# Kernel optimization log

Measured on AMD Instinct MI355X. Metric: run time of the kernel, lower is better.

## Reference

```python
import jax, jax.numpy as jnp
import numpy as np

N_ATOM, N_FRAG, N_EDGE, N_FEDGE, N_MEM = 131072, 32768, 262144, 65536, 196608
B, H, IN_A, IN_F, IN_E, L, OUT = 4096, 256, 64, 32, 16, 4, 1


def setup_inputs():
    ks = iter(jax.random.split(jax.random.key(0), 96))

    def nrm(shape, s=0.05):
        return jax.random.normal(next(ks), shape, jnp.float32) * s

    def ri(shape, hi):
        return jax.random.randint(next(ks), shape, 0, hi)

    z = lambda *s: jnp.zeros(s, jnp.float32)
    o = lambda *s: jnp.ones(s, jnp.float32)
    return {
        'x': nrm((N_ATOM, IN_A), 1.0),
        'fragments': nrm((N_FRAG, IN_F), 1.0),
        'edge_attr': nrm((N_EDGE, IN_E), 1.0),
        'atom_enc_W': nrm((IN_A, H)), 'atom_enc_b': z(H),
        'frag_enc_W': nrm((IN_F, H)), 'frag_enc_b': z(H),
        'bond_W': nrm((L, IN_E, H)), 'bond_b': z(L, H),
        'gine_eps': z(L),
        'gine_W1': nrm((L, H, 2 * H)), 'gine_b1': z(L, 2 * H),
        'gine_bn_g': o(L, 2 * H), 'gine_bn_b': z(L, 2 * H),
        'gine_W2': nrm((L, 2 * H, H)), 'gine_b2': z(L, H),
        'atom_bn_g': o(L, H), 'atom_bn_b': z(L, H),
        'gin_eps': z(L),
        'gin_W1': nrm((L, H, 2 * H)), 'gin_b1': z(L, 2 * H),
        'gin_bn_g': o(L, 2 * H), 'gin_bn_b': z(L, 2 * H),
        'gin_W2': nrm((L, 2 * H, H)), 'gin_b2': z(L, H),
        'frag_bn_g': o(L, H), 'frag_bn_b': z(L, H),
        'a2f_W': nrm((L, H, H)), 'a2f_b': z(L, H),
        'f2a_W': nrm((L, H, H)), 'f2a_b': z(L, H),
        'fo_W1': nrm((H, H)), 'fo_b1': z(H), 'fo_W2': nrm((H, H)), 'fo_b2': z(H),
        'ao_W1': nrm((H, H)), 'ao_b1': z(H), 'ao_W2': nrm((H, H)), 'ao_b2': z(H),
        'out_W1': nrm((H, H)), 'out_b1': z(H), 'out_W2': nrm((H, OUT)), 'out_b2': z(OUT),
        'edge_index': ri((2, N_EDGE), N_ATOM),
        'frag_edge_index': ri((2, N_FEDGE), N_FRAG),
        'batch': jnp.sort(ri((N_ATOM,), B)),
        'fragments_batch': jnp.sort(ri((N_FRAG,), B)),
        'mem_atom': ri((N_MEM,), N_ATOM),
        'mem_frag': ri((N_MEM,), N_FRAG),
    }


def _bn(x, g, b):
    # training-mode BatchNorm1d over the node dimension
    m = x.mean(0)
    v = jnp.mean((x - m) ** 2, 0)
    return (x - m) * jax.lax.rsqrt(v + 1e-5) * g + b


def _seg_sum(v, i, n):
    return jax.ops.segment_sum(v, i, num_segments=n)


def _seg_mean(v, i, n):
    s = _seg_sum(v, i, n)
    c = _seg_sum(jnp.ones((v.shape[0], 1), v.dtype), i, n)
    return s / jnp.maximum(c, 1.0)


def _forward(x, fragments, edge_attr, atom_enc_W, atom_enc_b, frag_enc_W, frag_enc_b, bond_W, bond_b, gine_eps, gine_W1, gine_b1, gine_bn_g, gine_bn_b, gine_W2, gine_b2, atom_bn_g, atom_bn_b, gin_eps, gin_W1, gin_b1, gin_bn_g, gin_bn_b, gin_W2, gin_b2, frag_bn_g, frag_bn_b, a2f_W, a2f_b, f2a_W, f2a_b, fo_W1, fo_b1, fo_W2, fo_b2, ao_W1, ao_b1, ao_W2, ao_b2, out_W1, out_b1, out_W2, out_b2, edge_index, frag_edge_index, batch, fragments_batch, mem_atom, mem_frag):
    a = x @ atom_enc_W + atom_enc_b            # [N_ATOM, H] atom encoder
    f = fragments @ frag_enc_W + frag_enc_b    # [N_FRAG, H] clique encoder
    src, dst = edge_index[0], edge_index[1]
    fsrc, fdst = frag_edge_index[0], frag_edge_index[1]
    n_atom, n_frag = a.shape[0], f.shape[0]
    for l in range(L):
        # per-layer bond encoder (learned_edge_rep=False)
        e = edge_attr @ bond_W[l] + bond_b[l]
        # GINEConv: sum_j relu(x_j + e_ij) gathered to target i
        agg = _seg_sum(jax.nn.relu(a[src] + e), dst, n_atom)
        h = (1.0 + gine_eps[l]) * a + agg
        h = jax.nn.relu(_bn(h @ gine_W1[l] + gine_b1[l], gine_bn_g[l], gine_bn_b[l]))
        a = jax.nn.relu(_bn(h @ gine_W2[l] + gine_b2[l], atom_bn_g[l], atom_bn_b[l]))
        # fragment GINConv on fragment graph
        fagg = _seg_sum(f[fsrc], fdst, n_frag)
        hf = (1.0 + gin_eps[l]) * f + fagg
        hf = jax.nn.relu(_bn(hf @ gin_W1[l] + gin_b1[l], gin_bn_g[l], gin_bn_b[l]))
        f = jax.nn.relu(_bn(hf @ gin_W2[l] + gin_b2[l], frag_bn_g[l], frag_bn_b[l]))
        # inter message passing over atom-fragment membership edges (mean reduce)
        f = f + _seg_mean(jax.nn.relu(a[mem_atom] @ a2f_W[l] + a2f_b[l]), mem_frag, n_frag)
        a = a + _seg_mean(jax.nn.relu(f[mem_frag] @ f2a_W[l] + f2a_b[l]), mem_atom, n_atom)
    # graph-level readout (mean pooling per molecule)
    fp = _seg_mean(f, fragments_batch, B)
    fp = jax.nn.relu(jax.nn.relu(fp @ fo_W1 + fo_b1) @ fo_W2 + fo_b2)
    ap = _seg_mean(a, batch, B)
    ap = jax.nn.relu(jax.nn.relu(ap @ ao_W1 + ao_b1) @ ao_W2 + ao_b2)
    zz = ap + fp
    return jax.nn.relu(zz @ out_W1 + out_b1) @ out_W2 + out_b2  # [B, OUT]


def reference(x, fragments, edge_attr, atom_enc_W, atom_enc_b, frag_enc_W, frag_enc_b, bond_W, bond_b, gine_eps, gine_W1, gine_b1, gine_bn_g, gine_bn_b, gine_W2, gine_b2, atom_bn_g, atom_bn_b, gin_eps, gin_W1, gin_b1, gin_bn_g, gin_bn_b, gin_W2, gin_b2, frag_bn_g, frag_bn_b, a2f_W, a2f_b, f2a_W, f2a_b, fo_W1, fo_b1, fo_W2, fo_b2, ao_W1, ao_b1, ao_W2, ao_b2, out_W1, out_b1, out_W2, out_b2, edge_index, frag_edge_index, batch, fragments_batch, mem_atom, mem_frag):
    return _forward(x, fragments, edge_attr, atom_enc_W, atom_enc_b, frag_enc_W, frag_enc_b, bond_W, bond_b, gine_eps, gine_W1, gine_b1, gine_bn_g, gine_bn_b, gine_W2, gine_b2, atom_bn_g, atom_bn_b, gin_eps, gin_W1, gin_b1, gin_bn_g, gin_bn_b, gin_W2, gin_b2, frag_bn_g, frag_bn_b, a2f_W, a2f_b, f2a_W, f2a_b, fo_W1, fo_b1, fo_W2, fo_b2, ao_W1, ao_b1, ao_W2, ao_b2, out_W1, out_b1, out_W2, out_b2, edge_index, frag_edge_index, batch, fragments_batch, mem_atom, mem_frag)
```

## Files before the change

### kernel.cpp

```cpp
#include <hip/hip_runtime.h>

#define CDIV(a,b) (((a)+(b)-1)/(b))

static const int N_ATOM = 131072, N_FRAG = 32768, N_EDGE = 262144,
                 N_FEDGE = 65536, N_MEM = 196608, BATCH = 4096, H = 256;
static const int NREP = 16;

typedef unsigned short ushort_t;
typedef _Float16 half8_t __attribute__((ext_vector_type(8)));
typedef float    floatx4 __attribute__((ext_vector_type(4)));

struct PanelsIn  { const ushort_t* p[4]; };
struct PanelsOut { ushort_t* p[4]; };

__device__ __forceinline__ float h2f(ushort_t u) {
    _Float16 h; __builtin_memcpy(&h, &u, 2); return (float)h;
}
__device__ __forceinline__ ushort_t f2h(float f) {
    _Float16 h = (_Float16)f; ushort_t u; __builtin_memcpy(&u, &h, 2); return u;
}

__device__ __forceinline__ void load_lds16(const ushort_t* g, ushort_t* l) {
    __builtin_amdgcn_global_load_lds(
        (const __attribute__((address_space(1))) unsigned int*)g,
        (__attribute__((address_space(3))) unsigned int*)l, 16, 0, 0);
}

__global__ void fill_const(float* p, long n, float v) {
    long t = (long)blockIdx.x * blockDim.x + threadIdx.x;
    long stride = (long)gridDim.x * blockDim.x;
    for (; t < n; t += stride) p[t] = v;
}

__global__ void prep_w(const float* __restrict__ s0, const float* __restrict__ s1,
                       const float* __restrict__ s2, const float* __restrict__ s3,
                       const float* __restrict__ s4, const float* __restrict__ s5,
                       ushort_t* __restrict__ hi, ushort_t* __restrict__ lo)
{
    long gid = (long)blockIdx.x * 256 + threadIdx.x;
    const float* src; int K, M; long base, loc;
    if      (gid < 524288)  { src=s0; K=256; M=512; base=0;       loc=gid; }
    else if (gid < 1048576) { src=s1; K=512; M=256; base=524288;  loc=gid-524288; }
    else if (gid < 1572864) { src=s2; K=256; M=512; base=1048576; loc=gid-1048576; }
    else if (gid < 2097152) { src=s3; K=512; M=256; base=1572864; loc=gid-1572864; }
    else if (gid < 2359296) { src=s4; K=256; M=256; base=2097152; loc=gid-2097152; }
    else if (gid < 2621440) { src=s5; K=256; M=256; base=2359296; loc=gid-2359296; }
    else return;
    long msz = (long)K * M;
    int  mat = (int)(loc / msz); long rem = loc - (long)mat * msz;
    int  k = (int)(rem / M);     int  n = (int)(rem - (long)k * M);
    float v = src[loc];
    ushort_t hu = f2h(v);
    ushort_t lu = f2h(v - h2f(hu));
    int nl = n & 127, g = (k >> 3) & 3;
    long p = (long)((nl >> 4) * 64 + g * 16 + (nl & 15));
    long dst = base + (long)mat * msz + (long)(k >> 5) * ((long)M << 5)
             + ((long)(n >> 7) << 12) + (p << 3) + (k & 7);
    hi[dst] = hu;
    if (lo) lo[dst] = lu;
}

template<int RELU>
__global__ __launch_bounds__(256)
void mfma_gemm(PanelsIn Ap, int astride, const ushort_t* __restrict__ Wh,
               const ushort_t* __restrict__ Wl, const float* __restrict__ bias,
               PanelsOut Cp, int cstride, const float* __restrict__ Aff,
               float* __restrict__ cstatR, int N, int K, int M)
{
    __shared__ ushort_t Asm[4096];
    __shared__ ushort_t Bhs[4096];
    __shared__ ushort_t Bls[4096];
    __shared__ ushort_t AffS[1024];
    const int tid = threadIdx.x;
    const int brow = blockIdx.y * 128, bcol = blockIdx.x * 128;
    const int wid = tid >> 6, lane = tid & 63;
    const int wm = wid >> 1, wn = wid & 1;
    const int lg = lane >> 4, lr = lane & 15;

    if (Aff) {
        for (int c = tid; c < K; c += 256) {
            AffS[c]       = f2h(Aff[c]);
            AffS[512 + c] = f2h(Aff[K + c]);
        }
        __syncthreads();
    }

    const int mA = lane & 15;
    const int gA = (lane >> 4) & 3;

    floatx4 acc[4][4];
    #pragma unroll
    for (int i = 0; i < 4; ++i)
        #pragma unroll
        for (int j = 0; j < 4; ++j) acc[i][j] = (floatx4){0.f, 0.f, 0.f, 0.f};

    const int nkt = K >> 5;
    for (int kt = 0; kt < nkt; ++kt) {
        if (kt) __syncthreads();
        const ushort_t* pa = Ap.p[kt >> 2];
        const ushort_t* ga = pa + (long)(brow + wid * 16 + mA) * astride
                                + ((kt & 3) << 5) + gA * 8;
        load_lds16(ga, Asm + wid * 512);
        load_lds16(ga + (long)64 * astride, Asm + 2048 + wid * 512);
        const ushort_t* gb = Wh + (size_t)kt * ((size_t)M << 5)
                                + ((size_t)bcol << 5) + (wid * 64 + lane) * 8;
        load_lds16(gb, Bhs + wid * 512);
        load_lds16(gb + 2048, Bhs + 2048 + wid * 512);
        if (Wl) {
            const ushort_t* gl = Wl + (size_t)kt * ((size_t)M << 5)
                                    + ((size_t)bcol << 5) + (wid * 64 + lane) * 8;
            load_lds16(gl, Bls + wid * 512);
            load_lds16(gl + 2048, Bls + 2048 + wid * 512);
        }
        __syncthreads();

        half8_t af[4], bh[4], bl[4];
        #pragma unroll
        for (int i = 0; i < 4; ++i)
            af[i] = *(const half8_t*)(Asm + (((wm * 4 + i) * 64 + lg * 16 + lr) << 3));
        if (Aff) {
            half8_t scv = *(const half8_t*)(AffS + (kt << 5) + lg * 8);
            half8_t sbv = *(const half8_t*)(AffS + 512 + (kt << 5) + lg * 8);
            #pragma unroll
            for (int i = 0; i < 4; ++i) {
                half8_t z = af[i] * scv + sbv;
                #pragma unroll
                for (int e = 0; e < 8; ++e)
                    z[e] = z[e] > (_Float16)0 ? z[e] : (_Float16)0;
                af[i] = z;
            }
        }
        #pragma unroll
        for (int j = 0; j < 4; ++j) {
            bh[j] = *(const half8_t*)(Bhs + (((wn * 4 + j) * 64 + lg * 16 + lr) << 3));
            if (Wl)
                bl[j] = *(const half8_t*)(Bls + (((wn * 4 + j) * 64 + lg * 16 + lr) << 3));
        }
        #pragma unroll
        for (int i = 0; i < 4; ++i)
            #pragma unroll
            for (int j = 0; j < 4; ++j) {
                acc[i][j] = __builtin_amdgcn_mfma_f32_16x16x32_f16(af[i], bh[j], acc[i][j], 0, 0, 0);
                if (Wl)
                    acc[i][j] = __builtin_amdgcn_mfma_f32_16x16x32_f16(af[i], bl[j], acc[i][j], 0, 0, 0);
            }
    }

    ushort_t* cb = Cp.p[blockIdx.x];
    float csl[4], cql[4];
    #pragma unroll
    for (int j = 0; j < 4; ++j) { csl[j] = 0.f; cql[j] = 0.f; }
    #pragma unroll
    for (int j = 0; j < 4; ++j) {
        int lcol = wn * 64 + j * 16 + lr;
        float bia = bias[bcol + lcol];
        #pragma unroll
        for (int i = 0; i < 4; ++i) {
            #pragma unroll
            for (int r = 0; r < 4; ++r) {
                int row = brow + wm * 64 + i * 16 + (lg << 2) + r;
                float v = acc[i][j][r] + bia;
                if (RELU) v = fmaxf(v, 0.f);
                ushort_t uo = f2h(v);
                cb[(long)row * cstride + lcol] = uo;
                if (cstatR) {
                    float vq = h2f(uo);
                    csl[j] += vq; cql[j] = fmaf(vq, vq, cql[j]);
                }
            }
        }
    }
    if (cstatR) {
        __syncthreads();
        float* cs = (float*)Asm;
        float* cq = (float*)Bhs;
        if (tid < 128) { cs[tid] = 0.f; cq[tid] = 0.f; }
        __syncthreads();
        #pragma unroll
        for (int j = 0; j < 4; ++j) {
            int cl = wn * 64 + j * 16 + lr;
            atomicAdd(&cs[cl], csl[j]);
            atomicAdd(&cq[cl], cql[j]);
        }
        __syncthreads();
        if (tid < 128) {
            int rep = blockIdx.y & (NREP - 1);
            atomicAdd(&cstatR[(long)rep * 2 * M + bcol + tid], cs[tid]);
            atomicAdd(&cstatR[(long)rep * 2 * M + M + bcol + tid], cq[tid]);
        }
    }
}

__global__ void finalize_aff(const float* __restrict__ cstatR, int M, float invN,
                             const float* __restrict__ g, const float* __restrict__ b,
                             float* __restrict__ aff)
{
    int c = blockIdx.x * blockDim.x + threadIdx.x;
    if (c >= M) return;
    float s = 0.f, q = 0.f;
    for (int r = 0; r < NREP; ++r) {
        s += cstatR[(long)r * 2 * M + c];
        q += cstatR[(long)r * 2 * M + M + c];
    }
    float m = s * invN, var = q * invN - m * m;
    float sa = rsqrtf(var + 1e-5f) * g[c];
    aff[c] = sa; aff[M + c] = b[c] - m * sa;
}

template<int EB>
__global__ __launch_bounds__(256)
void csr_agg(const ushort_t* __restrict__ in, ushort_t* __restrict__ out,
             const int* __restrict__ offs, const int* __restrict__ elist,
             const int* __restrict__ esrc, const float* __restrict__ eattr,
             const float* __restrict__ Wb, const float* __restrict__ bb,
             const float* __restrict__ eps_p, int n_nodes)
{
    __shared__ float Ws[EB ? 4096 : 1];
    __shared__ float bs[EB ? 256 : 1];
    if (EB) {
        for (int i = threadIdx.x; i < 4096; i += 256) Ws[i] = Wb[i];
        bs[threadIdx.x] = bb[threadIdx.x];
        __syncthreads();
    }
    float epsv = 1.f + eps_p[0];
    int lane = threadIdx.x & 63;
    int gw = (blockIdx.x * 256 + threadIdx.x) >> 6;
    int nw = (gridDim.x * 256) >> 6;
    for (int u = gw; u < n_nodes; u += nw) {
        const ushort_t* own = in + (long)u * 256;
        float acc[4];
        #pragma unroll
        for (int j = 0; j < 4; ++j) acc[j] = epsv * h2f(own[lane + 64 * j]);
        int s = offs[u], e = offs[u + 1];
        for (int i = s; i < e; ++i) {
            int eid = elist[i];
            int sid = esrc[eid];
            const ushort_t* row = in + (long)sid * 256;
            if (EB) {
                float ev[16];
                const float4* ea = (const float4*)(eattr + (long)eid * 16);
                float4 e0 = ea[0], e1 = ea[1], e2 = ea[2], e3 = ea[3];
                ev[0]=e0.x; ev[1]=e0.y; ev[2]=e0.z; ev[3]=e0.w;
                ev[4]=e1.x; ev[5]=e1.y; ev[6]=e1.z; ev[7]=e1.w;
                ev[8]=e2.x; ev[9]=e2.y; ev[10]=e2.z; ev[11]=e2.w;
                ev[12]=e3.x; ev[13]=e3.y; ev[14]=e3.z; ev[15]=e3.w;
                #pragma unroll
                for (int j = 0; j < 4; ++j) {
                    int c = lane + 64 * j;
                    float m = bs[c];
                    #pragma unroll
                    for (int k = 0; k < 16; ++k) m = fmaf(ev[k], Ws[k * 256 + c], m);
                    acc[j] += fmaxf(h2f(row[c]) + m, 0.f);
                }
            } else {
                #pragma unroll
                for (int j = 0; j < 4; ++j) acc[j] += h2f(row[lane + 64 * j]);
            }
        }
        ushort_t* o = out + (long)u * 256;
        #pragma unroll
        for (int j = 0; j < 4; ++j) o[lane + 64 * j] = f2h(acc[j]);
    }
}

__global__ __launch_bounds__(128)
void csr_mean_aff(const ushort_t* __restrict__ raw, const ushort_t* __restrict__ U,
                  const int* __restrict__ midx, const int* __restrict__ elist,
                  const int* __restrict__ offs, const float* __restrict__ Aff,
                  ushort_t* __restrict__ outp)
{
    int u = blockIdx.x, t = threadIdx.x;
    int c0 = t * 2;
    float sa0 = Aff[c0], sa1 = Aff[c0 + 1], sb0 = Aff[256 + c0], sb1 = Aff[256 + c0 + 1];
    ushort2 b = *(const ushort2*)(raw + (long)u * 256 + c0);
    float x0 = fmaxf(h2f(b.x) * sa0 + sb0, 0.f);
    float x1 = fmaxf(h2f(b.y) * sa1 + sb1, 0.f);
    int s = offs[u], e = offs[u + 1];
    float a0 = 0.f, a1 = 0.f;
    for (int i = s; i < e; ++i) {
        long r = midx[elist[i]];
        ushort2 v = *(const ushort2*)(U + r * 256 + c0);
        a0 += h2f(v.x); a1 += h2f(v.y);
    }
    if (e > s) { float inv = 1.f / (float)(e - s); x0 += a0 * inv; x1 += a1 * inv; }
    ushort2 o; o.x = f2h(x0); o.y = f2h(x1);
    *(ushort2*)(outp + (long)u * 256 + c0) = o;
}

template<int RELU, typename TC>
__global__ __launch_bounds__(256)
void gemm_k(const float* __restrict__ A, const float* __restrict__ W,
            const float* __restrict__ bias, TC* __restrict__ C,
            int N, int K, int M)
{
    const int BK = 16, LDA = 132;
    __shared__ float As[BK * LDA];
    __shared__ float Bs[BK * LDA];
    const int brow = blockIdx.y * 128;
    const int bcol = blockIdx.x * 128;
    const int tid  = threadIdx.x;
    const int tr = tid >> 4, tc = tid & 15;

    float acc[8][8];
    #pragma unroll
    for (int i = 0; i < 8; ++i)
        #pragma unroll
        for (int j = 0; j < 8; ++j) acc[i][j] = 0.f;

    for (int k0 = 0; k0 < K; k0 += BK) {
        #pragma unroll
        for (int u = 0; u < 8; ++u) {
            int idx = tid + u * 256;
            int m = idx >> 4, kk = idx & 15;
            As[kk * LDA + m] = A[(long)(brow + m) * K + k0 + kk];
        }
        #pragma unroll
        for (int u = 0; u < 8; ++u) {
            int idx = tid + u * 256;
            int kk = idx >> 7, n = idx & 127;
            int col = bcol + n;
            Bs[kk * LDA + n] = (col < M) ? W[(long)(k0 + kk) * M + col] : 0.f;
        }
        __syncthreads();
        #pragma unroll
        for (int kk = 0; kk < BK; ++kk) {
            float av[8], bv[8];
            float4 a0 = *(const float4*)&As[kk * LDA + tr * 8];
            float4 a1 = *(const float4*)&As[kk * LDA + tr * 8 + 4];
            float4 b0 = *(const float4*)&Bs[kk * LDA + tc * 8];
            float4 b1 = *(const float4*)&Bs[kk * LDA + tc * 8 + 4];
            av[0]=a0.x; av[1]=a0.y; av[2]=a0.z; av[3]=a0.w;
            av[4]=a1.x; av[5]=a1.y; av[6]=a1.z; av[7]=a1.w;
            bv[0]=b0.x; bv[1]=b0.y; bv[2]=b0.z; bv[3]=b0.w;
            bv[4]=b1.x; bv[5]=b1.y; bv[6]=b1.z; bv[7]=b1.w;
            #pragma unroll
            for (int i = 0; i < 8; ++i)
                #pragma unroll
                for (int j = 0; j < 8; ++j)
                    acc[i][j] = fmaf(av[i], bv[j], acc[i][j]);
        }
        __syncthreads();
    }
    #pragma unroll
    for (int i = 0; i < 8; ++i) {
        int row = brow + tr * 8 + i;
        #pragma unroll
        for (int j = 0; j < 8; ++j) {
            int col = bcol + tc * 8 + j;
            if (col < M) {
                float v = acc[i][j] + bias[col];
                if (RELU) v = fmaxf(v, 0.f);
                if constexpr (sizeof(TC) == 2) ((ushort_t*)C)[(long)row * M + col] = f2h(v);
                else                           ((float*)C)[(long)row * M + col] = v;
            }
        }
    }
}

__global__ void count_idx(const int* __restrict__ idx, int n, int* __restrict__ cnt)
{
    int i = blockIdx.x * blockDim.x + threadIdx.x;
    if (i < n) atomicAdd(&cnt[idx[i]], 1);
}

__global__ __launch_bounds__(256)
void scan_p1(const int* __restrict__ cnt, int n, int* __restrict__ partials)
{
    __shared__ int sd[256];
    int i = blockIdx.x * 256 + threadIdx.x;
    sd[threadIdx.x] = (i < n) ? cnt[i] : 0;
    __syncthreads();
    #pragma unroll
    for (int s = 128; s > 0; s >>= 1) {
        if (threadIdx.x < s) sd[threadIdx.x] += sd[threadIdx.x + s];
        __syncthreads();
    }
    if (threadIdx.x == 0) partials[blockIdx.x] = sd[0];
}

__global__ __launch_bounds__(1024)
void scan_p2(int* __restrict__ partials, int nb, int* __restrict__ off, int n)
{
    __shared__ int sd[1024];
    int t = threadIdx.x;
    int v = (t < nb) ? partials[t] : 0;
    sd[t] = v;
    __syncthreads();
    for (int d = 1; d < 1024; d <<= 1) {
        int x = (t >= d) ? sd[t - d] : 0;
        __syncthreads();
        sd[t] += x;
        __syncthreads();
    }
    if (t < nb) partials[t] = sd[t] - v;
    if (t == 1023) off[n] = sd[nb - 1];
}

__global__ __launch_bounds__(256)
void scan_p3(const int* __restrict__ cnt, int n, const int* __restrict__ partials,
             int* __restrict__ off, int* __restrict__ cursor)
{
    __shared__ int sd[256];
    int i = blockIdx.x * 256 + threadIdx.x;
    int v = (i < n) ? cnt[i] : 0;
    sd[threadIdx.x] = v;
    __syncthreads();
    for (int d = 1; d < 256; d <<= 1) {
        int x = (threadIdx.x >= d) ? sd[threadIdx.x - d] : 0;
        __syncthreads();
        sd[threadIdx.x] += x;
        __syncthreads();
    }
    if (i < n) {
        int e = partials[blockIdx.x] + sd[threadIdx.x] - v;
        off[i] = e; cursor[i] = e;
    }
}

__global__ void csr_fill(const int* __restrict__ idx, int n,
                         int* __restrict__ cursor, int* __restrict__ elist)
{
    int i = blockIdx.x * blockDim.x + threadIdx.x;
    if (i < n) { int p = atomicAdd(&cursor[idx[i]], 1); elist[p] = i; }
}

__global__ __launch_bounds__(256)
void seg_pool(const ushort_t* __restrict__ X, const int* __restrict__ bidx,
              int nrows, float* __restrict__ pooled)
{
    int b = blockIdx.x, t = threadIdx.x;
    int lo = 0, hi = nrows;
    while (lo < hi) { int mid = (lo + hi) >> 1; if (bidx[mid] < b) lo = mid + 1; else hi = mid; }
    int s = lo; hi = nrows;
    while (lo < hi) { int mid = (lo + hi) >> 1; if (bidx[mid] < b + 1) lo = mid + 1; else hi = mid; }
    int e = lo;
    float acc = 0.f;
    for (int r = s; r < e; ++r) acc += h2f(X[(long)r * 256 + t]);
    pooled[(long)b * 256 + t] = acc / fmaxf((float)(e - s), 1.f);
}

__global__ void vadd(float* __restrict__ out, const float* __restrict__ in, long n4)
{
    long t = (long)blockIdx.x * blockDim.x + threadIdx.x;
    if (t >= n4) return;
    float4 a = ((float4*)out)[t];
    float4 b = ((const float4*)in)[t];
    a.x += b.x; a.y += b.y; a.z += b.z; a.w += b.w;
    ((float4*)out)[t] = a;
}

extern "C" void kernel_launch(void* const* d_in, const int* in_sizes, int n_in,
                              void* d_out, int out_size, void* d_ws, size_t ws_size,
                              hipStream_t stream)
{
    (void)in_sizes; (void)n_in;
    const float* x          = (const float*)d_in[0];
    const float* fragments  = (const float*)d_in[1];
    const float* edge_attr  = (const float*)d_in[2];
    const float* atom_enc_W = (const float*)d_in[3];
    const float* atom_enc_b = (const float*)d_in[4];
    const float* frag_enc_W = (const float*)d_in[5];
    const float* frag_enc_b = (const float*)d_in[6];
    const float* bond_W     = (const float*)d_in[7];
    const float* bond_b     = (const float*)d_in[8];
    const float* gine_eps   = (const float*)d_in[9];
    const float* gine_W1    = (const float*)d_in[10];
    const float* gine_b1    = (const float*)d_in[11];
    const float* gine_bn_g  = (const float*)d_in[12];
    const float* gine_bn_b  = (const float*)d_in[13];
    const float* gine_W2    = (const float*)d_in[14];
    const float* gine_b2    = (const float*)d_in[15];
    const float* atom_bn_g  = (const float*)d_in[16];
    const float* atom_bn_b  = (const float*)d_in[17];
    const float* gin_eps    = (const float*)d_in[18];
    const float* gin_W1     = (const float*)d_in[19];
    const float* gin_b1     = (const float*)d_in[20];
    const float* gin_bn_g   = (const float*)d_in[21];
    const float* gin_bn_b   = (const float*)d_in[22];
    const float* gin_W2     = (const float*)d_in[23];
    const float* gin_b2     = (const float*)d_in[24];
    const float* frag_bn_g  = (const float*)d_in[25];
    const float* frag_bn_b  = (const float*)d_in[26];
    const float* a2f_W      = (const float*)d_in[27];
    const float* a2f_b      = (const float*)d_in[28];
    const float* f2a_W      = (const float*)d_in[29];
    const float* f2a_b      = (const float*)d_in[30];
    const float* fo_W1      = (const float*)d_in[31];
    const float* fo_b1      = (const float*)d_in[32];
    const float* fo_W2      = (const float*)d_in[33];
    const float* fo_b2      = (const float*)d_in[34];
    const float* ao_W1      = (const float*)d_in[35];
    const float* ao_b1      = (const float*)d_in[36];
    const float* ao_W2      = (const float*)d_in[37];
    const float* ao_b2      = (const float*)d_in[38];
    const float* out_W1     = (const float*)d_in[39];
    const float* out_b1     = (const float*)d_in[40];
    const float* out_W2     = (const float*)d_in[41];
    const float* out_b2     = (const float*)d_in[42];
    const int* edge_index   = (const int*)d_in[43];
    const int* fedge_index  = (const int*)d_in[44];
    const int* batch        = (const int*)d_in[45];
    const int* fbatch       = (const int*)d_in[46];
    const int* mem_atom     = (const int*)d_in[47];
    const int* mem_frag     = (const int*)d_in[48];

    const int* src  = edge_index;
    const int* dst  = edge_index + N_EDGE;
    const int* fsrc = fedge_index;
    const int* fdst = fedge_index + N_FEDGE;

    size_t off = 0;
    auto take = [&](size_t b) -> size_t { size_t p = off; off = (off + b + 255) & ~(size_t)255; return p; };
    size_t o_big   = take((size_t)N_ATOM * 512 * 2);
    size_t o_a     = take((size_t)N_ATOM * H * 2);
    size_t o_f     = take((size_t)N_FRAG * H * 2);
    size_t o_f2    = take((size_t)N_FRAG * H * 2);
    size_t o_offea = take((size_t)(N_ATOM + 1) * 4);
    size_t o_elea  = take((size_t)N_EDGE * 4);
    size_t o_offef = take((size_t)(N_FRAG + 1) * 4);
    size_t o_elef  = take((size_t)N_FEDGE * 4);
    size_t o_offma = take((size_t)(N_ATOM + 1) * 4);
    size_t o_elma  = take((size_t)N_MEM * 4);
    size_t o_offmf = take((size_t)(N_FRAG + 1) * 4);
    size_t o_elmf  = take((size_t)N_MEM * 4);
    size_t o_cnta  = take((size_t)N_ATOM * 4);
    size_t o_cntf  = take((size_t)N_FRAG * 4);
    size_t o_part  = take(1024 * 4);
    size_t o_stats = take((size_t)NREP * 3072 * 4);
    size_t o_aff   = take(3072 * 4);
    size_t o_hi    = take((size_t)2621440 * 2);
    size_t need_nolo = off;
    size_t o_lo    = take((size_t)2621440 * 2);
    size_t need_full = off;

    bool use_lo = (need_full <= ws_size);
    if (!use_lo && need_nolo > ws_size) {
        fill_const<<<64, 256, 0, stream>>>((float*)d_out, out_size,
                                           (float)((double)ws_size / 1024.0));
        return;
    }
    char* base = (char*)d_ws;
    char*     big     = base + o_big;
    ushort_t* a       = (ushort_t*)(base + o_a);
    ushort_t* f       = (ushort_t*)(base + o_f);
    ushort_t* f2      = (ushort_t*)(base + o_f2);
    int* off_ea = (int*)(base + o_offea);
    int* el_ea  = (int*)(base + o_elea);
    int* off_ef = (int*)(base + o_offef);
    int* el_ef  = (int*)(base + o_elef);
    int* off_ma = (int*)(base + o_offma);
    int* el_ma  = (int*)(base + o_elma);
    int* off_mf = (int*)(base + o_offmf);
    int* el_mf  = (int*)(base + o_elmf);
    int* cnt_a  = (int*)(base + o_cnta);
    int* cnt_f  = (int*)(base + o_cntf);
    int* parts  = (int*)(base + o_part);
    float* statsR = (float*)(base + o_stats);
    float* affs   = (float*)(base + o_aff);
    ushort_t* Wp_hi = (ushort_t*)(base + o_hi);
    ushort_t* Wp_lo = use_lo ? (ushort_t*)(base + o_lo) : nullptr;

    float* cst1a = statsR;
    float* cst2a = statsR + (size_t)NREP * 1024;
    float* cst1f = statsR + (size_t)NREP * 1536;
    float* cst2f = statsR + (size_t)NREP * 2560;
    float* aff1_a = affs;
    float* aff2_a = affs + 1024;
    float* aff1_f = affs + 1536;
    float* aff2_f = affs + 2560;

    ushort_t* big_u = (ushort_t*)big;
    const size_t HALF_U = (size_t)N_ATOM * 256;
    ushort_t* ha  = big_u + HALF_U;
    const size_t PAN_A = (size_t)N_ATOM * 128;
    const size_t PAN_F = (size_t)N_FRAG * 128;
    ushort_t* Ua = big_u;
    float* pooled_f = (float*)big;
    float* pooled_a = (float*)(big + (size_t)8 * 1024 * 1024);
    float* tmp      = (float*)(big + (size_t)16 * 1024 * 1024);

    const long WG0 = 0, WG1 = 524288, WG2 = 1048576, WG3 = 1572864,
               WG4 = 2097152, WG5 = 2359296;

    auto build_csr = [&](const int* idx, int n_edges, int n_nodes,
                         int* cnt, int* offs, int* elist) {
        hipMemsetAsync(cnt, 0, (size_t)n_nodes * 4, stream);
        count_idx<<<CDIV(n_edges,256),256,0,stream>>>(idx, n_edges, cnt);
        int nb = CDIV(n_nodes, 256);
        scan_p1<<<nb, 256, 0, stream>>>(cnt, n_nodes, parts);
        scan_p2<<<1, 1024, 0, stream>>>(parts, nb, offs, n_nodes);
        scan_p3<<<nb, 256, 0, stream>>>(cnt, n_nodes, parts, offs, cnt);
        csr_fill<<<CDIV(n_edges,256),256,0,stream>>>(idx, n_edges, cnt, elist);
    };

    prep_w<<<CDIV(2621440L, 256), 256, 0, stream>>>(gine_W1, gine_W2, gin_W1, gin_W2,
                                                    a2f_W, f2a_W, Wp_hi, Wp_lo);
    build_csr(dst,      N_EDGE,  N_ATOM, cnt_a, off_ea, el_ea);
    build_csr(fdst,     N_FEDGE, N_FRAG, cnt_f, off_ef, el_ef);
    build_csr(mem_atom, N_MEM,   N_ATOM, cnt_a, off_ma, el_ma);
    build_csr(mem_frag, N_MEM,   N_FRAG, cnt_f, off_mf, el_mf);

    gemm_k<0,ushort_t><<<dim3(2, N_ATOM/128), 256, 0, stream>>>(
        x, atom_enc_W, atom_enc_b, a, N_ATOM, 64, H);
    gemm_k<0,ushort_t><<<dim3(2, N_FRAG/128), 256, 0, stream>>>(
        fragments, frag_enc_W, frag_enc_b, f, N_FRAG, 32, H);

    const float invNA = 1.f / N_ATOM, invNF = 1.f / N_FRAG;

    for (int l = 0; l < 4; ++l) {
        hipMemsetAsync(statsR, 0, (size_t)NREP * 3072 * 4, stream);

        csr_agg<1><<<2048, 256, 0, stream>>>(a, ha, off_ea, el_ea, src, edge_attr,
            bond_W + (long)l*16*H, bond_b + l*H, gine_eps + l, N_ATOM);

        PanelsIn A1in; PanelsOut A1out;
        for (int i = 0; i < 4; ++i) A1in.p[i] = ha + i * 128;
        A1out.p[0] = a;          A1out.p[1] = a + PAN_A;
        A1out.p[2] = big_u;      A1out.p[3] = big_u + PAN_A;
        mfma_gemm<0><<<dim3(4, N_ATOM/128), 256, 0, stream>>>(
            A1in, 256, Wp_hi + WG0 + (long)l*131072,
            Wp_lo ? Wp_lo + WG0 + (long)l*131072 : nullptr,
            gine_b1 + l*512, A1out, 128, nullptr, cst1a, N_ATOM, 256, 512);
        finalize_aff<<<2, 256, 0, stream>>>(cst1a, 512, invNA,
            gine_bn_g + l*512, gine_bn_b + l*512, aff1_a);

        PanelsIn A2in; PanelsOut A2out;
        A2in.p[0] = a;       A2in.p[1] = a + PAN_A;
        A2in.p[2] = big_u;   A2in.p[3] = big_u + PAN_A;
        A2out.p[0] = ha; A2out.p[1] = ha + 128; A2out.p[2] = ha; A2out.p[3] = ha;
        mfma_gemm<0><<<dim3(2, N_ATOM/128), 256, 0, stream>>>(
            A2in, 128, Wp_hi + WG1 + (long)l*131072,
            Wp_lo ? Wp_lo + WG1 + (long)l*131072 : nullptr,
            gine_b2 + l*H, A2out, 256, aff1_a, cst2a, N_ATOM, 512, 256);
        finalize_aff<<<1, 256, 0, stream>>>(cst2a, 256, invNA,
            atom_bn_g + l*H, atom_bn_b + l*H, aff2_a);

        csr_agg<0><<<512, 256, 0, stream>>>(f, f2, off_ef, el_ef, fsrc, nullptr,
            nullptr, nullptr, gin_eps + l, N_FRAG);

        PanelsIn F1in; PanelsOut F1out;
        for (int i = 0; i < 4; ++i) F1in.p[i] = f2 + i * 128;
        for (int i = 0; i < 4; ++i) F1out.p[i] = big_u + i * PAN_F;
        mfma_gemm<0><<<dim3(4, N_FRAG/128), 256, 0, stream>>>(
            F1in, 256, Wp_hi + WG2 + (long)l*131072,
            Wp_lo ? Wp_lo + WG2 + (long)l*131072 : nullptr,
            gin_b1 + l*512, F1out, 128, nullptr, cst1f, N_FRAG, 256, 512);
        finalize_aff<<<2, 256, 0, stream>>>(cst1f, 512, invNF,
            gin_bn_g + l*512, gin_bn_b + l*512, aff1_f);

        PanelsIn F2in; PanelsOut F2out;
        for (int i = 0; i < 4; ++i) F2in.p[i] = big_u + i * PAN_F;
        F2out.p[0] = f2; F2out.p[1] = f2 + 128; F2out.p[2] = f2; F2out.p[3] = f2;
        mfma_gemm<0><<<dim3(2, N_FRAG/128), 256, 0, stream>>>(
            F2in, 128, Wp_hi + WG3 + (long)l*131072,
            Wp_lo ? Wp_lo + WG3 + (long)l*131072 : nullptr,
            gin_b2 + l*H, F2out, 256, aff1_f, cst2f, N_FRAG, 512, 256);
        finalize_aff<<<1, 256, 0, stream>>>(cst2f, 256, invNF,
            frag_bn_g + l*H, frag_bn_b + l*H, aff2_f);

        PanelsIn UAin; PanelsOut UAout;
        for (int i = 0; i < 4; ++i) UAin.p[i] = ha + i * 128;
        UAout.p[0] = Ua; UAout.p[1] = Ua + 128; UAout.p[2] = Ua; UAout.p[3] = Ua;
        mfma_gemm<1><<<dim3(2, N_ATOM/128), 256, 0, stream>>>(
            UAin, 256, Wp_hi + WG4 + (long)l*65536,
            Wp_lo ? Wp_lo + WG4 + (long)l*65536 : nullptr,
            a2f_b + l*H, UAout, 256, aff2_a, nullptr, N_ATOM, 256, 256);
        csr_mean_aff<<<N_FRAG, 128, 0, stream>>>(f2, Ua, mem_atom, el_mf, off_mf,
                                                 aff2_f, f);
        PanelsIn UFin; PanelsOut UFout;
        for (int i = 0; i < 4; ++i) UFin.p[i] = f + i * 128;
        UFout.p[0] = f2; UFout.p[1] = f2 + 128; UFout.p[2] = f2; UFout.p[3] = f2;
        mfma_gemm<1><<<dim3(2, N_FRAG/128), 256, 0, stream>>>(
            UFin, 256, Wp_hi + WG5 + (long)l*65536,
            Wp_lo ? Wp_lo + WG5 + (long)l*65536 : nullptr,
            f2a_b + l*H, UFout, 256, nullptr, nullptr, N_FRAG, 256, 256);
        csr_mean_aff<<<N_ATOM, 128, 0, stream>>>(ha, f2, mem_frag, el_ma, off_ma,
                                                 aff2_a, a);
    }

    seg_pool<<<BATCH, 256, 0, stream>>>(f, fbatch, N_FRAG, pooled_f);
    gemm_k<1,float><<<dim3(2, BATCH/128), 256, 0, stream>>>(
        pooled_f, fo_W1, fo_b1, tmp, BATCH, H, H);
    gemm_k<1,float><<<dim3(2, BATCH/128), 256, 0, stream>>>(
        tmp, fo_W2, fo_b2, pooled_f, BATCH, H, H);

    seg_pool<<<BATCH, 256, 0, stream>>>(a, batch, N_ATOM, pooled_a);
    gemm_k<1,float><<<dim3(2, BATCH/128), 256, 0, stream>>>(
        pooled_a, ao_W1, ao_b1, tmp, BATCH, H, H);
    gemm_k<1,float><<<dim3(2, BATCH/128), 256, 0, stream>>>(
        tmp, ao_W2, ao_b2, pooled_a, BATCH, H, H);

    vadd<<<(int)CDIV((long)BATCH*H/4,256), 256, 0, stream>>>(
        pooled_a, pooled_f, (long)BATCH * H / 4);
    gemm_k<1,float><<<dim3(2, BATCH/128), 256, 0, stream>>>(
        pooled_a, out_W1, out_b1, tmp, BATCH, H, H);
    gemm_k<0,float><<<dim3(1, BATCH/128), 256, 0, stream>>>(
        tmp, out_W2, out_b2, (float*)d_out, BATCH, H, 1);
}
```

Measured before the change: 3.638 ms.

## Move encoder GEMMs to MFMA path and drop lo-weight correction for a2f/f2a

Converts x and fragments to fp16 and runs the atom/fragment encoders through the packed MFMA GEMM, with their weights added to the prep_w panel packing, replacing the scalar fp32 gemm_k. It also passes a null lo-weight pointer for the a2f and f2a GEMMs, skipping the split-precision correction pass there. A third change pads the gemm_k LDS stride. These cut FP32 SIMT work and MFMA work, at the cost of lower precision from fp16 inputs and hi-only weights.

```diff
diff --git a/kernel.cpp b/kernel.cpp
--- a/kernel.cpp
+++ b/kernel.cpp
@@ -32,9 +32,21 @@
     for (; t < n; t += stride) p[t] = v;
 }
 
+__global__ void conv_f2h(const float* __restrict__ in, ushort_t* __restrict__ out, long n)
+{
+    long t = (long)blockIdx.x * 256 + threadIdx.x;
+    long stride = (long)gridDim.x * 256;
+    for (long i = t; i < n / 4; i += stride) {
+        float4 v = ((const float4*)in)[i];
+        ushort4 o; o.x = f2h(v.x); o.y = f2h(v.y); o.z = f2h(v.z); o.w = f2h(v.w);
+        ((ushort4*)out)[i] = o;
+    }
+}
+
 __global__ void prep_w(const float* __restrict__ s0, const float* __restrict__ s1,
                        const float* __restrict__ s2, const float* __restrict__ s3,
                        const float* __restrict__ s4, const float* __restrict__ s5,
+                       const float* __restrict__ s6, const float* __restrict__ s7,
                        ushort_t* __restrict__ hi, ushort_t* __restrict__ lo)
 {
     long gid = (long)blockIdx.x * 256 + threadIdx.x;
@@ -45,6 +57,8 @@
     else if (gid < 2097152) { src=s3; K=512; M=256; base=1572864; loc=gid-1572864; }
     else if (gid < 2359296) { src=s4; K=256; M=256; base=2097152; loc=gid-2097152; }
     else if (gid < 2621440) { src=s5; K=256; M=256; base=2359296; loc=gid-2359296; }
+    else if (gid < 2637824) { src=s6; K=64;  M=256; base=2621440; loc=gid-2621440; }
+    else if (gid < 2646016) { src=s7; K=32;  M=256; base=2637824; loc=gid-2637824; }
     else return;
     long msz = (long)K * M;
     int  mat = (int)(loc / msz); long rem = loc - (long)mat * msz;
@@ -293,7 +307,7 @@
             const float* __restrict__ bias, TC* __restrict__ C,
             int N, int K, int M)
 {
-    const int BK = 16, LDA = 132;
+    const int BK = 16, LDA = 133;
     __shared__ float As[BK * LDA];
     __shared__ float Bs[BK * LDA];
     const int brow = blockIdx.y * 128;
@@ -509,6 +523,7 @@
     const int* fsrc = fedge_index;
     const int* fdst = fedge_index + N_FEDGE;
 
+    const size_t WPN = 2646016;
     size_t off = 0;
     auto take = [&](size_t b) -> size_t { size_t p = off; off = (off + b + 255) & ~(size_t)255; return p; };
     size_t o_big   = take((size_t)N_ATOM * 512 * 2);
@@ -528,9 +543,9 @@
     size_t o_part  = take(1024 * 4);
     size_t o_stats = take((size_t)NREP * 3072 * 4);
     size_t o_aff   = take(3072 * 4);
-    size_t o_hi    = take((size_t)2621440 * 2);
+    size_t o_hi    = take(WPN * 2);
     size_t need_nolo = off;
-    size_t o_lo    = take((size_t)2621440 * 2);
+    size_t o_lo    = take(WPN * 2);
     size_t need_full = off;
 
     bool use_lo = (need_full <= ws_size);
@@ -578,9 +593,11 @@
     float* pooled_f = (float*)big;
     float* pooled_a = (float*)(big + (size_t)8 * 1024 * 1024);
     float* tmp      = (float*)(big + (size_t)16 * 1024 * 1024);
+    ushort_t* xh = big_u;
+    ushort_t* fh = big_u + (size_t)N_ATOM * 64;
 
     const long WG0 = 0, WG1 = 524288, WG2 = 1048576, WG3 = 1572864,
-               WG4 = 2097152, WG5 = 2359296;
+               WG4 = 2097152, WG5 = 2359296, WG6 = 2621440, WG7 = 2637824;
 
     auto build_csr = [&](const int* idx, int n_edges, int n_nodes,
                          int* cnt, int* offs, int* elist) {
@@ -593,17 +610,30 @@
         csr_fill<<<CDIV(n_edges,256),256,0,stream>>>(idx, n_edges, cnt, elist);
     };
 
-    prep_w<<<CDIV(2621440L, 256), 256, 0, stream>>>(gine_W1, gine_W2, gin_W1, gin_W2,
-                                                    a2f_W, f2a_W, Wp_hi, Wp_lo);
+    prep_w<<<CDIV((long)WPN, 256), 256, 0, stream>>>(gine_W1, gine_W2, gin_W1, gin_W2,
+                                                     a2f_W, f2a_W, atom_enc_W, frag_enc_W,
+                                                     Wp_hi, Wp_lo);
     build_csr(dst,      N_EDGE,  N_ATOM, cnt_a, off_ea, el_ea);
     build_csr(fdst,     N_FEDGE, N_FRAG, cnt_f, off_ef, el_ef);
     build_csr(mem_atom, N_MEM,   N_ATOM, cnt_a, off_ma, el_ma);
     build_csr(mem_frag, N_MEM,   N_FRAG, cnt_f, off_mf, el_mf);
 
-    gemm_k<0,ushort_t><<<dim3(2, N_ATOM/128), 256, 0, stream>>>(
-        x, atom_enc_W, atom_enc_b, a, N_ATOM, 64, H);
-    gemm_k<0,ushort_t><<<dim3(2, N_FRAG/128), 256, 0, stream>>>(
-        fragments, frag_enc_W, frag_enc_b, f, N_FRAG, 32, H);
+    conv_f2h<<<2048, 256, 0, stream>>>(x, xh, (long)N_ATOM * 64);
+    conv_f2h<<<512, 256, 0, stream>>>(fragments, fh, (long)N_FRAG * 32);
+    {
+        PanelsIn Ein; PanelsOut Eout;
+        for (int i = 0; i < 4; ++i) Ein.p[i] = xh;
+        Eout.p[0] = a; Eout.p[1] = a + 128; Eout.p[2] = a; Eout.p[3] = a;
+        mfma_gemm<0><<<dim3(2, N_ATOM/128), 256, 0, stream>>>(
+            Ein, 64, Wp_hi + WG6, Wp_lo ? Wp_lo + WG6 : nullptr,
+            atom_enc_b, Eout, 256, nullptr, nullptr, N_ATOM, 64, 256);
+        PanelsIn Fin; PanelsOut Fout;
+        for (int i = 0; i < 4; ++i) Fin.p[i] = fh;
+        Fout.p[0] = f; Fout.p[1] = f + 128; Fout.p[2] = f; Fout.p[3] = f;
+        mfma_gemm<0><<<dim3(2, N_FRAG/128), 256, 0, stream>>>(
+            Fin, 32, Wp_hi + WG7, Wp_lo ? Wp_lo + WG7 : nullptr,
+            frag_enc_b, Fout, 256, nullptr, nullptr, N_FRAG, 32, 256);
+    }
 
     const float invNA = 1.f / N_ATOM, invNF = 1.f / N_FRAG;
 
@@ -662,8 +692,7 @@
         for (int i = 0; i < 4; ++i) UAin.p[i] = ha + i * 128;
         UAout.p[0] = Ua; UAout.p[1] = Ua + 128; UAout.p[2] = Ua; UAout.p[3] = Ua;
         mfma_gemm<1><<<dim3(2, N_ATOM/128), 256, 0, stream>>>(
-            UAin, 256, Wp_hi + WG4 + (long)l*65536,
-            Wp_lo ? Wp_lo + WG4 + (long)l*65536 : nullptr,
+            UAin, 256, Wp_hi + WG4 + (long)l*65536, nullptr,
             a2f_b + l*H, UAout, 256, aff2_a, nullptr, N_ATOM, 256, 256);
         csr_mean_aff<<<N_FRAG, 128, 0, stream>>>(f2, Ua, mem_atom, el_mf, off_mf,
                                                  aff2_f, f);
@@ -671,8 +700,7 @@
         for (int i = 0; i < 4; ++i) UFin.p[i] = f + i * 128;
         UFout.p[0] = f2; UFout.p[1] = f2 + 128; UFout.p[2] = f2; UFout.p[3] = f2;
         mfma_gemm<1><<<dim3(2, N_FRAG/128), 256, 0, stream>>>(
-            UFin, 256, Wp_hi + WG5 + (long)l*65536,
-            Wp_lo ? Wp_lo + WG5 + (long)l*65536 : nullptr,
+            UFin, 256, Wp_hi + WG5 + (long)l*65536, nullptr,
             f2a_b + l*H, UFout, 256, nullptr, nullptr, N_FRAG, 256, 256);
         csr_mean_aff<<<N_ATOM, 128, 0, stream>>>(ha, f2, mem_frag, el_ma, off_ma,
                                                  aff2_a, a);
```

Measured after the change: 3.475 ms. 4.5% less time.
